# Performance work log

Hardware: AMD Instinct MI355X
Metric: run time of the kernel (lower is better)

Reference implementation:

```python
import jax, jax.numpy as jnp
import numpy as np

# DARTS recurrent genotype (canonical): (activation, predecessor-state index)
GENOTYPE_RECURRENT = [("sigmoid", 0), ("relu", 1), ("relu", 1), ("identity", 1),
                      ("tanh", 2), ("sigmoid", 5), ("tanh", 3), ("relu", 5)]
GENOTYPE_CONCAT = [1, 2, 3, 4, 5, 6, 7, 8]

T, B, H, V = 512, 64, 1024, 50000
INITRANGE = 0.04

_ACT = {"tanh": jnp.tanh, "relu": jax.nn.relu, "sigmoid": jax.nn.sigmoid,
        "identity": lambda x: x}


def setup_inputs() -> dict:
    key = jax.random.key(0)
    ks = jax.random.split(key, 5)
    X = jax.random.randint(ks[0], (T, B), 0, V)                     # token ids (T, B)
    hidden = jnp.zeros((1, B, H), dtype=jnp.float32)                # init hidden list[0]
    emb_table = jax.random.normal(ks[1], (V, H), dtype=jnp.float32) * 0.1
    W0 = jax.random.uniform(ks[2], (2 * H, 2 * H), jnp.float32, -INITRANGE, INITRANGE)
    Ws = jax.random.uniform(ks[3], (len(GENOTYPE_RECURRENT), H, 2 * H), jnp.float32,
                            -INITRANGE, INITRANGE)
    W_out = jax.random.normal(ks[4], (H, 4), dtype=jnp.float32) * 0.02
    b_out = jnp.zeros((4,), dtype=jnp.float32)
    return {"X": X, "hidden": hidden, "emb_table": emb_table, "W0": W0,
            "Ws": Ws, "W_out": W_out, "b_out": b_out}


def _darts_cell_step(h_prev, x, W0, Ws):
    # x, h_prev: (B, H). Eval-mode (no dropout masks).
    xh = jnp.concatenate([x, h_prev], axis=-1)          # (B, 2H)
    c0h0 = xh @ W0                                      # (B, 2H)
    c0 = jax.nn.sigmoid(c0h0[:, :H])
    h0 = jnp.tanh(c0h0[:, H:])
    s0 = h_prev + c0 * (h0 - h_prev)
    states = [s0]
    for i, (name, pred) in enumerate(GENOTYPE_RECURRENT):
        s_prev = states[pred]
        ch = s_prev @ Ws[i]                             # (B, 2H)
        c = jax.nn.sigmoid(ch[:, :H])
        hh = _ACT[name](ch[:, H:])
        states.append(s_prev + c * (hh - s_prev))
    # mean over concat nodes
    out = jnp.mean(jnp.stack([states[i] for i in GENOTYPE_CONCAT], axis=-1), axis=-1)
    return out, out


def reference(X, hidden, emb_table, W0, Ws, W_out, b_out):
    emb = emb_table[X]                                  # (T, B, H)
    h0 = hidden[0]                                      # (B, H)

    def step(h, x_t):
        return _darts_cell_step(h, x_t, W0, Ws)

    h_last, hiddens = jax.lax.scan(step, h0, emb)       # h_last: (B, H)
    a_hat = h_last @ W_out + b_out                      # (B, 4)
    probs = jax.nn.softmax(a_hat, axis=1)
    return a_hat, probs
```

## Files before the change

### kernel.cpp

```cpp
#include <hip/hip_runtime.h>

#define TT 512

typedef _Float16 f16;
typedef _Float16 half8 __attribute__((ext_vector_type(8)));
typedef float f32x4 __attribute__((ext_vector_type(4)));

#define MFMA(a,b,c) __builtin_amdgcn_mfma_f32_16x16x32_f16((a),(b),(c),0,0,0)
#define LOSC  2048.0f
#define RLOSC 0.00048828125f

#define RS  18
#define WSZ (16*RS)
#define LSZ (16*WSZ)

__device__ __forceinline__ half8 ldh8(const f16* p){ return *(const half8*)p; }
__device__ __forceinline__ float sgm(float x){ return 1.f/(1.f+__expf(-x)); }
__device__ __forceinline__ float applyact(int k, float x){
  if (k==0) return tanhf(x);
  if (k==1) return sgm(x);
  if (k==2) return fmaxf(x,0.f);
  return x;
}

__device__ __forceinline__ void gbar_arrive(unsigned* bar, unsigned ph, int b, int tid){
  __syncthreads();
  if (tid==0){
    __builtin_amdgcn_fence(__ATOMIC_RELEASE, "agent");
    __hip_atomic_store(&bar[b*16], ph+1u, __ATOMIC_RELAXED, __HIP_MEMORY_SCOPE_AGENT);
  }
}

__device__ __forceinline__ void gbar_wait(unsigned* bar, unsigned ph, int b, int tid){
  const unsigned tgt = ph + 1u;
  if (b==0){
    if (tid<256){
      while (__hip_atomic_load(&bar[tid*16], __ATOMIC_RELAXED, __HIP_MEMORY_SCOPE_AGENT) < tgt)
        __builtin_amdgcn_s_sleep(2);
    }
    __syncthreads();
    if (tid==0){
      __builtin_amdgcn_fence(__ATOMIC_ACQ_REL, "agent");
      __hip_atomic_store(&bar[4096], tgt, __ATOMIC_RELAXED, __HIP_MEMORY_SCOPE_AGENT);
    }
  }
  if (tid==0){
    while (__hip_atomic_load(&bar[4096], __ATOMIC_RELAXED, __HIP_MEMORY_SCOPE_AGENT) < tgt)
      __builtin_amdgcn_s_sleep(2);
    __builtin_amdgcn_fence(__ATOMIC_ACQUIRE, "agent");
  }
  __syncthreads();
}

struct WF2 { half8 g0,a0,gl0,al0,g1,a1,gl1,al1; };

__device__ __forceinline__ WF2 preW(const f16* __restrict__ Wh, const f16* __restrict__ Wl,
  int Kst, int c0, int kk, int q8, int l15, int wlo)
{
  WF2 F;
  const f16* Bg = Wh + (size_t)(c0+l15)*Kst + kk + q8;
  const f16* Ba = Wh + (size_t)(1024+c0+l15)*Kst + kk + q8;
  F.g0=ldh8(Bg); F.a0=ldh8(Ba); F.g1=ldh8(Bg+32); F.a1=ldh8(Ba+32);
  if (wlo){
    const f16* Bgl = Wl + (size_t)(c0+l15)*Kst + kk + q8;
    const f16* Bal = Wl + (size_t)(1024+c0+l15)*Kst + kk + q8;
    F.gl0=ldh8(Bgl); F.al0=ldh8(Bal); F.gl1=ldh8(Bgl+32); F.al1=ldh8(Bal+32);
  } else { F.gl0=F.g0; F.al0=F.a0; F.gl1=F.g1; F.al1=F.a1; }
  return F;
}

template<int NCH>
__device__ __forceinline__ void mm_mix(const WF2& F,
  const f16* __restrict__ Ap, const f16* __restrict__ Alp,
  const f16* __restrict__ Bg, const f16* __restrict__ Ba,
  const f16* __restrict__ Bgl, const f16* __restrict__ Bal,
  int wlo, float* __restrict__ Lg, float* __restrict__ La,
  int region, int q8, int l15)
{
  f32x4 g0={0,0,0,0},g1={0,0,0,0},a0={0,0,0,0},a1={0,0,0,0};
  {
    half8 ah=ldh8(Ap), al=ldh8(Alp);
    g0=MFMA(ah,F.g0,g0); a0=MFMA(ah,F.a0,a0);
    g1=MFMA(al,F.g0,g1); a1=MFMA(al,F.a0,a1);
    if (wlo){ g1=MFMA(ah,F.gl0,g1); a1=MFMA(ah,F.al0,a1); }
  }
  if (NCH>1){
    half8 ah=ldh8(Ap+32), al=ldh8(Alp+32);
    g0=MFMA(ah,F.g1,g0); a0=MFMA(ah,F.a1,a0);
    g1=MFMA(al,F.g1,g1); a1=MFMA(al,F.a1,a1);
    if (wlo){ g1=MFMA(ah,F.gl1,g1); a1=MFMA(ah,F.al1,a1); }
  }
  #pragma unroll
  for (int c=2;c<NCH;c++){
    int s=c*32;
    half8 ah=ldh8(Ap+s), al=ldh8(Alp+s);
    half8 wg=ldh8(Bg+s), wa=ldh8(Ba+s);
    g0=MFMA(ah,wg,g0); a0=MFMA(ah,wa,a0);
    g1=MFMA(al,wg,g1); a1=MFMA(al,wa,a1);
    if (wlo){ g1=MFMA(ah,ldh8(Bgl+s),g1); a1=MFMA(ah,ldh8(Bal+s),a1); }
  }
  f32x4 gg = g0 + g1*RLOSC, aa = a0 + a1*RLOSC;
  const int base = region*WSZ + (q8>>1)*RS + l15;
  #pragma unroll
  for (int rr=0;rr<4;rr++){
    Lg[base + rr*RS] = gg[rr];
    La[base + rr*RS] = aa[rr];
  }
}

template<int NCH>
__device__ __forceinline__ void node_pre(const WF2& F,
  const f16* __restrict__ SHs, const f16* __restrict__ SLs,
  const f16* __restrict__ Wh, const f16* __restrict__ Wl,
  float* __restrict__ Lg, float* __restrict__ La,
  int region, int kk, int m0, int c0, int q8, int l15, int wlo)
{
  const f16* Ap  = SHs + (m0+l15)*1024 + kk + q8;
  const f16* Alp = SLs + (m0+l15)*1024 + kk + q8;
  const f16* Bg  = Wh + (size_t)(c0+l15)*1024 + kk + q8;
  const f16* Ba  = Wh + (size_t)(1024+c0+l15)*1024 + kk + q8;
  const f16* Bgl = wlo ? Wl + (size_t)(c0+l15)*1024 + kk + q8 : Bg;
  const f16* Bal = wlo ? Wl + (size_t)(1024+c0+l15)*1024 + kk + q8 : Ba;
  mm_mix<NCH>(F, Ap, Alp, Bg, Ba, Bgl, Bal, wlo, Lg, La, region, q8, l15);
}

__device__ __forceinline__ float fin_val(const float* __restrict__ Lg, const float* __restrict__ La,
  const float* __restrict__ ST, int t256, int m0, int c0, int r0, int nr, int sp, int actk)
{
  const int row = t256>>4, col = t256&15;
  const int e = row*RS + col;
  float gs=0.f, as=0.f;
  for (int r=r0; r<r0+nr; ++r){ gs += Lg[r*WSZ+e]; as += La[r*WSZ+e]; }
  float spv = ST[sp*65536 + (m0+row)*1024 + c0 + col];
  return spv + sgm(gs)*(applyact(actk,as)-spv);
}

__device__ __forceinline__ void fin_write(const float* __restrict__ Lg, const float* __restrict__ La,
  float* __restrict__ ST, f16* __restrict__ SH, f16* __restrict__ SL,
  int t256, int m0, int c0, int r0, int nr, int sp, int so, int actk, bool hl)
{
  float s = fin_val(Lg, La, ST, t256, m0, c0, r0, nr, sp, actk);
  const int row = t256>>4, col = t256&15;
  const int idx = so*65536 + (m0+row)*1024 + c0 + col;
  ST[idx] = s;
  if (hl){ f16 hi=(f16)s; SH[idx]=hi; SL[idx]=(f16)((s-(float)hi)*LOSC); }
}

__global__ __launch_bounds__(1024,4) void darts_coop(
  const int* __restrict__ X, const float* __restrict__ emb,
  const float* __restrict__ Wout, const float* __restrict__ bout, float* __restrict__ out,
  const f16* __restrict__ W0Th, const f16* __restrict__ W0Tl,
  const f16* __restrict__ WsTh, const f16* __restrict__ WsTl,
  float* __restrict__ ST, f16* __restrict__ SH, f16* __restrict__ SL,
  f16* __restrict__ XNH, f16* __restrict__ XNL,
  unsigned* bar, int wlo)
{
  const int tid = threadIdx.x, b = blockIdx.x;
  const int wid = tid>>6, lane = tid&63, l15 = lane&15, q8 = (lane>>4)*8;
  const int mt = (b>>3)&3, sct = (b&7)*8 + (b>>5);
  const int m0 = mt*16, c0 = sct*16;
  __shared__ float Lg[LSZ], La[LSZ];
  __shared__ float S6[256], S8[256];
  unsigned ph = 0;

  WF2 F0 = preW(W0Th, W0Tl, 2048, c0, wid*128, q8, l15, wlo);

  for (int t=0; t<TT; ++t){
    if (t+1 < TT && tid < 256){
      int row = b>>2, col = ((b&3)<<8) + tid;
      int tok = X[(t+1)*64 + row];
      float v = emb[(size_t)tok*1024 + col];
      f16 hi=(f16)v;
      int xi = ((t+1)&1)*65536 + row*1024 + col;
      XNH[xi]=hi; XNL[xi]=(f16)((v-(float)hi)*LOSC);
    }
    {
      const f16* XH = XNH + (t&1)*65536;
      const f16* XL = XNL + (t&1)*65536;
      int kk = wid*128, ak = kk & 1023;
      const f16* Abh = (wid<8)? XH : SH;
      const f16* Abl = (wid<8)? XL : SL;
      const f16* Ap  = Abh + (m0+l15)*1024 + ak + q8;
      const f16* Alp = Abl + (m0+l15)*1024 + ak + q8;
      const f16* Bg  = W0Th + (size_t)(c0+l15)*2048 + kk + q8;
      const f16* Ba  = W0Th + (size_t)(1024+c0+l15)*2048 + kk + q8;
      const f16* Bgl = wlo ? W0Tl + (size_t)(c0+l15)*2048 + kk + q8 : Bg;
      const f16* Bal = wlo ? W0Tl + (size_t)(1024+c0+l15)*2048 + kk + q8 : Ba;
      mm_mix<4>(F0, Ap, Alp, Bg, Ba, Bgl, Bal, wlo, Lg, La, wid, q8, l15);
    }
    __syncthreads();
    if (tid<256) fin_write(Lg,La,ST,SH,SL, tid, m0,c0, 0,16, 0, 1, 0, true);
    gbar_arrive(bar, ph, b, tid);
    WF2 F1 = preW(WsTh, WsTl, 1024, c0, wid*64, q8, l15, wlo);
    gbar_wait(bar, ph, b, tid); ph++;

    node_pre<2>(F1, SH+1*65536, SL+1*65536, WsTh, WsTl, Lg, La, wid, wid*64, m0,c0,q8,l15,wlo);
    __syncthreads();
    if (tid<256) fin_write(Lg,La,ST,SH,SL, tid, m0,c0, 0,16, 1, 2, 1, true);
    gbar_arrive(bar, ph, b, tid);
    WF2 F2 = (wid<8)
      ? preW(WsTh+(size_t)1*2097152, wlo? WsTl+(size_t)1*2097152 : (const f16*)0,
             1024, c0, (wid&7)*128, q8, l15, wlo)
      : preW(WsTh+(size_t)2*2097152, wlo? WsTl+(size_t)2*2097152 : (const f16*)0,
             1024, c0, (wid&7)*128, q8, l15, wlo);
    gbar_wait(bar, ph, b, tid); ph++;

    if (wid<8)
      node_pre<4>(F2, SH+2*65536, SL+2*65536, WsTh+(size_t)1*2097152,
                  wlo? WsTl+(size_t)1*2097152 : (const f16*)0,
                  Lg, La, wid, (wid&7)*128, m0,c0,q8,l15,wlo);
    else
      node_pre<4>(F2, SH+2*65536, SL+2*65536, WsTh+(size_t)2*2097152,
                  wlo? WsTl+(size_t)2*2097152 : (const f16*)0,
                  Lg, La, wid, (wid&7)*128, m0,c0,q8,l15,wlo);
    __syncthreads();
    if (tid<256)      fin_write(Lg,La,ST,SH,SL, tid,     m0,c0, 0,8, 2, 3, 2, true);
    else if (tid<512) fin_write(Lg,La,ST,SH,SL, tid-256, m0,c0, 8,8, 2, 4, 2, true);
    __syncthreads();

    {
      WF2 F2b = preW(WsTh+(size_t)3*2097152, wlo? WsTl+(size_t)3*2097152 : (const f16*)0,
                     1024, c0, wid*64, q8, l15, wlo);
      node_pre<2>(F2b, SH+2*65536, SL+2*65536, WsTh+(size_t)3*2097152,
                  wlo? WsTl+(size_t)3*2097152 : (const f16*)0,
                  Lg, La, wid, wid*64, m0,c0,q8,l15,wlo);
    }
    __syncthreads();
    if (tid<256) fin_write(Lg,La,ST,SH,SL, tid, m0,c0, 0,16, 2, 5, 3, false);
    gbar_arrive(bar, ph, b, tid);
    WF2 F3 = (wid<8)
      ? preW(WsTh+(size_t)4*2097152, wlo? WsTl+(size_t)4*2097152 : (const f16*)0,
             1024, c0, (wid&7)*128, q8, l15, wlo)
      : preW(WsTh+(size_t)6*2097152, wlo? WsTl+(size_t)6*2097152 : (const f16*)0,
             1024, c0, (wid&7)*128, q8, l15, wlo);
    gbar_wait(bar, ph, b, tid); ph++;

    if (wid<8)
      node_pre<4>(F3, SH+3*65536, SL+3*65536, WsTh+(size_t)4*2097152,
                  wlo? WsTl+(size_t)4*2097152 : (const f16*)0,
                  Lg, La, wid, (wid&7)*128, m0,c0,q8,l15,wlo);
    else
      node_pre<4>(F3, SH+4*65536, SL+4*65536, WsTh+(size_t)6*2097152,
                  wlo? WsTl+(size_t)6*2097152 : (const f16*)0,
                  Lg, La, wid, (wid&7)*128, m0,c0,q8,l15,wlo);
    __syncthreads();
    if (tid<256)      fin_write(Lg,La,ST,SH,SL, tid,     m0,c0, 0,8, 3, 6, 0, true);
    else if (tid<512) fin_write(Lg,La,ST,SH,SL, tid-256, m0,c0, 8,8, 4, 8, 0, false);
    gbar_arrive(bar, ph, b, tid);
    WF2 F4 = (wid<8)
      ? preW(WsTh+(size_t)5*2097152, wlo? WsTl+(size_t)5*2097152 : (const f16*)0,
             1024, c0, (wid&7)*128, q8, l15, wlo)
      : preW(WsTh+(size_t)7*2097152, wlo? WsTl+(size_t)7*2097152 : (const f16*)0,
             1024, c0, (wid&7)*128, q8, l15, wlo);
    gbar_wait(bar, ph, b, tid); ph++;

    if (wid<8)
      node_pre<4>(F4, SH+6*65536, SL+6*65536, WsTh+(size_t)5*2097152,
                  wlo? WsTl+(size_t)5*2097152 : (const f16*)0,
                  Lg, La, wid, (wid&7)*128, m0,c0,q8,l15,wlo);
    else
      node_pre<4>(F4, SH+6*65536, SL+6*65536, WsTh+(size_t)7*2097152,
                  wlo? WsTl+(size_t)7*2097152 : (const f16*)0,
                  Lg, La, wid, (wid&7)*128, m0,c0,q8,l15,wlo);
    __syncthreads();
    if (tid<256)      S6[tid]     = fin_val(Lg,La,ST, tid,     m0,c0, 0,8, 6, 1);
    else if (tid<512) S8[tid-256] = fin_val(Lg,La,ST, tid-256, m0,c0, 8,8, 6, 2);
    __syncthreads();
    if (tid<256){
      const int row = tid>>4, col = tid&15;
      const int idx = (m0+row)*1024 + c0 + col;
      float m = (ST[2*65536+idx]+ST[3*65536+idx]+ST[4*65536+idx]+ST[5*65536+idx]
               + ST[6*65536+idx]+ST[8*65536+idx]+S6[tid]+S8[tid])*0.125f;
      ST[idx]=m;
      f16 hi=(f16)m; SH[idx]=hi; SL[idx]=(f16)((m-(float)hi)*LOSC);
    }
    gbar_arrive(bar, ph, b, tid);
    F0 = preW(W0Th, W0Tl, 2048, c0, wid*128, q8, l15, wlo);
    gbar_wait(bar, ph, b, tid); ph++;
  }

  if (b==0 && tid<256){
    int row = tid>>2, col = tid&3;
    float acc = bout[col];
    const float* hrow = ST + row*1024;
    #pragma unroll 8
    for (int k=0;k<1024;k++) acc += hrow[k]*Wout[k*4+col];
    out[row*4+col] = acc;
    float m = fmaxf(acc, __shfl_xor(acc,1));
    m = fmaxf(m, __shfl_xor(m,2));
    float e = __expf(acc-m);
    float ssum = e + __shfl_xor(e,1);
    ssum = ssum + __shfl_xor(ssum,2);
    out[256 + row*4+col] = e/ssum;
  }
}

__global__ void prep_x0(const int* __restrict__ X, const float* __restrict__ hidden,
  const float* __restrict__ emb, f16* __restrict__ XNH, f16* __restrict__ XNL,
  float* __restrict__ ST, f16* __restrict__ SH, f16* __restrict__ SL, unsigned* bar)
{
  int idx = blockIdx.x*256 + threadIdx.x;
  float hv = hidden[idx];
  ST[idx] = hv;
  f16 hh=(f16)hv; SH[idx]=hh; SL[idx]=(f16)((hv-(float)hh)*LOSC);
  int brow = idx>>10, k = idx&1023;
  int tok = X[brow];
  float v = emb[tok*1024+k];
  f16 xh=(f16)v; XNH[idx]=xh; XNL[idx]=(f16)((v-(float)xh)*LOSC);
  if (idx < 8192) bar[idx] = 0u;
}

__global__ void prep_w(const float* __restrict__ W0, const float* __restrict__ Ws,
  f16* __restrict__ W0Th, f16* __restrict__ W0Tl, f16* __restrict__ WsTh, f16* __restrict__ WsTl)
{
  __shared__ float L[64][65];
  int b = blockIdx.x, tid = threadIdx.x;
  const float* src; f16 *Dh, *Dl; int K, tk, tn;
  if (b < 1024){ src=W0; Dh=W0Th; Dl=W0Tl; K=2048; tk=b&31; tn=b>>5; }
  else { int bb=b-1024; int mi=bb>>9; int t2=bb&511; tk=t2&15; tn=t2>>4;
         src = Ws + (size_t)mi*1024*2048; Dh = WsTh + (size_t)mi*2097152;
         Dl = WsTl ? (WsTl + (size_t)mi*2097152) : (f16*)0; K=1024; }
  int k0 = tk*64, n0 = tn*64;
  int rr = tid>>6, cc = tid&63;
  #pragma unroll
  for (int j=0;j<16;j++){
    int r = j*4 + rr;
    L[cc][r] = src[(size_t)(k0+r)*2048 + n0+cc];
  }
  __syncthreads();
  #pragma unroll
  for (int j=0;j<16;j++){
    int n = j*4 + rr;
    float v = L[n][cc];
    f16 hi = (f16)v;
    Dh[(size_t)(n0+n)*K + k0+cc] = hi;
    if (Dl) Dl[(size_t)(n0+n)*K + k0+cc] = (f16)((v-(float)hi)*LOSC);
  }
}

__global__ void sentinel_k(float* __restrict__ out, float v){
  int i = blockIdx.x*256 + threadIdx.x;
  if (i < 512) out[i] = v;
}

extern "C" void kernel_launch(void* const* d_in, const int* in_sizes, int n_in,
                              void* d_out, int out_size, void* d_ws, size_t ws_size,
                              hipStream_t stream)
{
  const int*   X      = (const int*)  d_in[0];
  const float* hidden = (const float*)d_in[1];
  const float* emb    = (const float*)d_in[2];
  const float* W0     = (const float*)d_in[3];
  const float* Ws     = (const float*)d_in[4];
  const float* Wout   = (const float*)d_in[5];
  const float* bout   = (const float*)d_in[6];
  float* out = (float*)d_out;

  const size_t SZ_W0   = (size_t)2048*2048*2;
  const size_t SZ_WS   = (size_t)8*2048*1024*2;
  const size_t SZ_ST   = (size_t)10*65536*4;
  const size_t SZ_SHL  = (size_t)10*65536*2;
  const size_t SZ_XN   = (size_t)2*65536*2;
  const size_t SZ_BAR  = 32768;

  auto pad = [](size_t x){ return (x + 255) & ~(size_t)255; };
  size_t need_red  = pad(SZ_W0) + pad(SZ_WS) + pad(SZ_ST) + 2*pad(SZ_SHL)
                   + 2*pad(SZ_XN) + pad(SZ_BAR);
  size_t need_full = need_red + pad(SZ_W0) + pad(SZ_WS);

  int wlo;
  if (ws_size >= need_full)      wlo = 1;
  else if (ws_size >= need_red)  wlo = 0;
  else { hipLaunchKernelGGL(sentinel_k, dim3(2), dim3(256), 0, stream, out, 1.0e6f); return; }

  char* w = (char*)d_ws; size_t off = 0;
  auto alloc = [&](size_t bytes)->void*{ void* p = w+off; off += (bytes+255)&~(size_t)255; return p; };
  f16* W0Th = (f16*)alloc(SZ_W0);
  f16* WsTh = (f16*)alloc(SZ_WS);
  f16* W0Tl = wlo ? (f16*)alloc(SZ_W0) : (f16*)0;
  f16* WsTl = wlo ? (f16*)alloc(SZ_WS) : (f16*)0;
  float* ST = (float*)alloc(SZ_ST);
  f16* SH   = (f16*)alloc(SZ_SHL);
  f16* SL   = (f16*)alloc(SZ_SHL);
  f16* XNH  = (f16*)alloc(SZ_XN);
  f16* XNL  = (f16*)alloc(SZ_XN);
  unsigned* bar = (unsigned*)alloc(SZ_BAR);

  hipLaunchKernelGGL(prep_x0, dim3(256), dim3(256), 0, stream,
                     X, hidden, emb, XNH, XNL, ST, SH, SL, bar);
  hipLaunchKernelGGL(prep_w, dim3(5120), dim3(256), 0, stream,
                     W0, Ws, W0Th, W0Tl, WsTh, WsTl);

  void* args[] = { (void*)&X, (void*)&emb, (void*)&Wout, (void*)&bout, (void*)&out,
                   (void*)&W0Th, (void*)&W0Tl, (void*)&WsTh, (void*)&WsTl,
                   (void*)&ST, (void*)&SH, (void*)&SL, (void*)&XNH, (void*)&XNL,
                   (void*)&bar, (void*)&wlo };
  hipError_t e = hipLaunchCooperativeKernel((void*)darts_coop, dim3(256), dim3(1024), args, 0, stream);
  if (e != hipSuccess){
    hipLaunchKernelGGL(darts_coop, dim3(256), dim3(1024), 0, stream,
                       X, emb, Wout, bout, out, W0Th, W0Tl, WsTh, WsTl,
                       ST, SH, SL, XNH, XNL, bar, wlo);
  }
}
```

Measured before the change: 64.89 ms.

## Replace grid-barrier fences with sc1 coherent loads/stores and drop weight prefetch

Removes the agent-scope acquire/release fences from the grid barrier wait path. Shared state values are instead read and written with inline-asm global loads and stores carrying the sc1 cache-coherence bit, so they bypass non-coherent cache levels. The activation fragments are batch-issued before one waitcnt. The register-held weight prefetch that was overlapped with the barrier wait is removed, so weights are now loaded inside the matmul loop. This cuts cache-invalidate and writeback cost at each of the many barriers per step. The cost is losing weight-load overlap and depending on sc1 semantics for correctness, and the arrive-side release fence remains.

```diff
diff --git a/kernel.cpp b/kernel.cpp
--- a/kernel.cpp
+++ b/kernel.cpp
@@ -23,6 +23,24 @@
   return x;
 }
 
+__device__ __forceinline__ void issue_ld4_sc1(half8& d, const f16* p){
+  asm volatile("global_load_dwordx4 %0, %1, off sc1" : "=&v"(d) : "v"(p) : "memory");
+}
+__device__ __forceinline__ void issue_ldf_sc1(float& d, const float* p){
+  asm volatile("global_load_dword %0, %1, off sc1" : "=&v"(d) : "v"(p) : "memory");
+}
+__device__ __forceinline__ void vmwait(){
+  asm volatile("s_waitcnt vmcnt(0)" ::: "memory");
+  __builtin_amdgcn_sched_barrier(0);
+}
+__device__ __forceinline__ void st_f32_sc1(float* p, float v){
+  asm volatile("global_store_dword %0, %1, off sc1" :: "v"(p), "v"(v) : "memory");
+}
+__device__ __forceinline__ void st_f16_sc1(f16* p, f16 v){
+  unsigned uv = (unsigned)__builtin_bit_cast(unsigned short, v);
+  asm volatile("global_store_short %0, %1, off sc1" :: "v"(p), "v"(uv) : "memory");
+}
+
 __device__ __forceinline__ void gbar_arrive(unsigned* bar, unsigned ph, int b, int tid){
   __syncthreads();
   if (tid==0){
@@ -39,65 +57,39 @@
         __builtin_amdgcn_s_sleep(2);
     }
     __syncthreads();
-    if (tid==0){
-      __builtin_amdgcn_fence(__ATOMIC_ACQ_REL, "agent");
+    if (tid==0)
       __hip_atomic_store(&bar[4096], tgt, __ATOMIC_RELAXED, __HIP_MEMORY_SCOPE_AGENT);
-    }
   }
   if (tid==0){
     while (__hip_atomic_load(&bar[4096], __ATOMIC_RELAXED, __HIP_MEMORY_SCOPE_AGENT) < tgt)
       __builtin_amdgcn_s_sleep(2);
-    __builtin_amdgcn_fence(__ATOMIC_ACQUIRE, "agent");
   }
   __syncthreads();
 }
 
-struct WF2 { half8 g0,a0,gl0,al0,g1,a1,gl1,al1; };
-
-__device__ __forceinline__ WF2 preW(const f16* __restrict__ Wh, const f16* __restrict__ Wl,
-  int Kst, int c0, int kk, int q8, int l15, int wlo)
-{
-  WF2 F;
-  const f16* Bg = Wh + (size_t)(c0+l15)*Kst + kk + q8;
-  const f16* Ba = Wh + (size_t)(1024+c0+l15)*Kst + kk + q8;
-  F.g0=ldh8(Bg); F.a0=ldh8(Ba); F.g1=ldh8(Bg+32); F.a1=ldh8(Ba+32);
-  if (wlo){
-    const f16* Bgl = Wl + (size_t)(c0+l15)*Kst + kk + q8;
-    const f16* Bal = Wl + (size_t)(1024+c0+l15)*Kst + kk + q8;
-    F.gl0=ldh8(Bgl); F.al0=ldh8(Bal); F.gl1=ldh8(Bgl+32); F.al1=ldh8(Bal+32);
-  } else { F.gl0=F.g0; F.al0=F.a0; F.gl1=F.g1; F.al1=F.a1; }
-  return F;
-}
-
 template<int NCH>
-__device__ __forceinline__ void mm_mix(const WF2& F,
+__device__ __forceinline__ void mm_core(
   const f16* __restrict__ Ap, const f16* __restrict__ Alp,
   const f16* __restrict__ Bg, const f16* __restrict__ Ba,
   const f16* __restrict__ Bgl, const f16* __restrict__ Bal,
   int wlo, float* __restrict__ Lg, float* __restrict__ La,
   int region, int q8, int l15)
 {
+  half8 AH[NCH], AL[NCH];
+  #pragma unroll
+  for (int c=0;c<NCH;c++){
+    issue_ld4_sc1(AH[c], Ap+c*32);
+    issue_ld4_sc1(AL[c], Alp+c*32);
+  }
+  vmwait();
   f32x4 g0={0,0,0,0},g1={0,0,0,0},a0={0,0,0,0},a1={0,0,0,0};
-  {
-    half8 ah=ldh8(Ap), al=ldh8(Alp);
-    g0=MFMA(ah,F.g0,g0); a0=MFMA(ah,F.a0,a0);
-    g1=MFMA(al,F.g0,g1); a1=MFMA(al,F.a0,a1);
-    if (wlo){ g1=MFMA(ah,F.gl0,g1); a1=MFMA(ah,F.al0,a1); }
-  }
-  if (NCH>1){
-    half8 ah=ldh8(Ap+32), al=ldh8(Alp+32);
-    g0=MFMA(ah,F.g1,g0); a0=MFMA(ah,F.a1,a0);
-    g1=MFMA(al,F.g1,g1); a1=MFMA(al,F.a1,a1);
-    if (wlo){ g1=MFMA(ah,F.gl1,g1); a1=MFMA(ah,F.al1,a1); }
-  }
-  #pragma unroll
-  for (int c=2;c<NCH;c++){
-    int s=c*32;
-    half8 ah=ldh8(Ap+s), al=ldh8(Alp+s);
+  #pragma unroll
+  for (int c=0;c<NCH;c++){
+    int s = c*32;
     half8 wg=ldh8(Bg+s), wa=ldh8(Ba+s);
-    g0=MFMA(ah,wg,g0); a0=MFMA(ah,wa,a0);
-    g1=MFMA(al,wg,g1); a1=MFMA(al,wa,a1);
-    if (wlo){ g1=MFMA(ah,ldh8(Bgl+s),g1); a1=MFMA(ah,ldh8(Bal+s),a1); }
+    g0=MFMA(AH[c],wg,g0); a0=MFMA(AH[c],wa,a0);
+    g1=MFMA(AL[c],wg,g1); a1=MFMA(AL[c],wa,a1);
+    if (wlo){ g1=MFMA(AH[c],ldh8(Bgl+s),g1); a1=MFMA(AH[c],ldh8(Bal+s),a1); }
   }
   f32x4 gg = g0 + g1*RLOSC, aa = a0 + a1*RLOSC;
   const int base = region*WSZ + (q8>>1)*RS + l15;
@@ -109,7 +101,7 @@
 }
 
 template<int NCH>
-__device__ __forceinline__ void node_pre(const WF2& F,
+__device__ __forceinline__ void node_std(
   const f16* __restrict__ SHs, const f16* __restrict__ SLs,
   const f16* __restrict__ Wh, const f16* __restrict__ Wl,
   float* __restrict__ Lg, float* __restrict__ La,
@@ -121,17 +113,19 @@
   const f16* Ba  = Wh + (size_t)(1024+c0+l15)*1024 + kk + q8;
   const f16* Bgl = wlo ? Wl + (size_t)(c0+l15)*1024 + kk + q8 : Bg;
   const f16* Bal = wlo ? Wl + (size_t)(1024+c0+l15)*1024 + kk + q8 : Ba;
-  mm_mix<NCH>(F, Ap, Alp, Bg, Ba, Bgl, Bal, wlo, Lg, La, region, q8, l15);
+  mm_core<NCH>(Ap,Alp,Bg,Ba,Bgl,Bal,wlo,Lg,La,region,q8,l15);
 }
 
 __device__ __forceinline__ float fin_val(const float* __restrict__ Lg, const float* __restrict__ La,
   const float* __restrict__ ST, int t256, int m0, int c0, int r0, int nr, int sp, int actk)
 {
   const int row = t256>>4, col = t256&15;
+  float spv;
+  issue_ldf_sc1(spv, ST + sp*65536 + (m0+row)*1024 + c0 + col);
   const int e = row*RS + col;
   float gs=0.f, as=0.f;
   for (int r=r0; r<r0+nr; ++r){ gs += Lg[r*WSZ+e]; as += La[r*WSZ+e]; }
-  float spv = ST[sp*65536 + (m0+row)*1024 + c0 + col];
+  vmwait();
   return spv + sgm(gs)*(applyact(actk,as)-spv);
 }
 
@@ -142,8 +136,8 @@
   float s = fin_val(Lg, La, ST, t256, m0, c0, r0, nr, sp, actk);
   const int row = t256>>4, col = t256&15;
   const int idx = so*65536 + (m0+row)*1024 + c0 + col;
-  ST[idx] = s;
-  if (hl){ f16 hi=(f16)s; SH[idx]=hi; SL[idx]=(f16)((s-(float)hi)*LOSC); }
+  st_f32_sc1(ST+idx, s);
+  if (hl){ f16 hi=(f16)s; st_f16_sc1(SH+idx, hi); st_f16_sc1(SL+idx, (f16)((s-(float)hi)*LOSC)); }
 }
 
 __global__ __launch_bounds__(1024,4) void darts_coop(
@@ -163,8 +157,6 @@
   __shared__ float S6[256], S8[256];
   unsigned ph = 0;
 
-  WF2 F0 = preW(W0Th, W0Tl, 2048, c0, wid*128, q8, l15, wlo);
-
   for (int t=0; t<TT; ++t){
     if (t+1 < TT && tid < 256){
       int row = b>>2, col = ((b&3)<<8) + tid;
@@ -172,7 +164,8 @@
       float v = emb[(size_t)tok*1024 + col];
       f16 hi=(f16)v;
       int xi = ((t+1)&1)*65536 + row*1024 + col;
-      XNH[xi]=hi; XNL[xi]=(f16)((v-(float)hi)*LOSC);
+      st_f16_sc1(XNH+xi, hi);
+      st_f16_sc1(XNL+xi, (f16)((v-(float)hi)*LOSC));
     }
     {
       const f16* XH = XNH + (t&1)*65536;
@@ -186,31 +179,25 @@
       const f16* Ba  = W0Th + (size_t)(1024+c0+l15)*2048 + kk + q8;
       const f16* Bgl = wlo ? W0Tl + (size_t)(c0+l15)*2048 + kk + q8 : Bg;
       const f16* Bal = wlo ? W0Tl + (size_t)(1024+c0+l15)*2048 + kk + q8 : Ba;
-      mm_mix<4>(F0, Ap, Alp, Bg, Ba, Bgl, Bal, wlo, Lg, La, wid, q8, l15);
+      mm_core<4>(Ap,Alp,Bg,Ba,Bgl,Bal,wlo,Lg,La,wid,q8,l15);
     }
     __syncthreads();
     if (tid<256) fin_write(Lg,La,ST,SH,SL, tid, m0,c0, 0,16, 0, 1, 0, true);
     gbar_arrive(bar, ph, b, tid);
-    WF2 F1 = preW(WsTh, WsTl, 1024, c0, wid*64, q8, l15, wlo);
-    gbar_wait(bar, ph, b, tid); ph++;
-
-    node_pre<2>(F1, SH+1*65536, SL+1*65536, WsTh, WsTl, Lg, La, wid, wid*64, m0,c0,q8,l15,wlo);
+    gbar_wait(bar, ph, b, tid); ph++;
+
+    node_std<2>(SH+1*65536, SL+1*65536, WsTh, WsTl, Lg, La, wid, wid*64, m0,c0,q8,l15,wlo);
     __syncthreads();
     if (tid<256) fin_write(Lg,La,ST,SH,SL, tid, m0,c0, 0,16, 1, 2, 1, true);
     gbar_arrive(bar, ph, b, tid);
-    WF2 F2 = (wid<8)
-      ? preW(WsTh+(size_t)1*2097152, wlo? WsTl+(size_t)1*2097152 : (const f16*)0,
-             1024, c0, (wid&7)*128, q8, l15, wlo)
-      : preW(WsTh+(size_t)2*2097152, wlo? WsTl+(size_t)2*2097152 : (const f16*)0,
-             1024, c0, (wid&7)*128, q8, l15, wlo);
     gbar_wait(bar, ph, b, tid); ph++;
 
     if (wid<8)
-      node_pre<4>(F2, SH+2*65536, SL+2*65536, WsTh+(size_t)1*2097152,
+      node_std<4>(SH+2*65536, SL+2*65536, WsTh+(size_t)1*2097152,
                   wlo? WsTl+(size_t)1*2097152 : (const f16*)0,
                   Lg, La, wid, (wid&7)*128, m0,c0,q8,l15,wlo);
     else
-      node_pre<4>(F2, SH+2*65536, SL+2*65536, WsTh+(size_t)2*2097152,
+      node_std<4>(SH+2*65536, SL+2*65536, WsTh+(size_t)2*2097152,
                   wlo? WsTl+(size_t)2*2097152 : (const f16*)0,
                   Lg, La, wid, (wid&7)*128, m0,c0,q8,l15,wlo);
     __syncthreads();
@@ -218,48 +205,34 @@
     else if (tid<512) fin_write(Lg,La,ST,SH,SL, tid-256, m0,c0, 8,8, 2, 4, 2, true);
     __syncthreads();
 
-    {
-      WF2 F2b = preW(WsTh+(size_t)3*2097152, wlo? WsTl+(size_t)3*2097152 : (const f16*)0,
-                     1024, c0, wid*64, q8, l15, wlo);
-      node_pre<2>(F2b, SH+2*65536, SL+2*65536, WsTh+(size_t)3*2097152,
-                  wlo? WsTl+(size_t)3*2097152 : (const f16*)0,
-                  Lg, La, wid, wid*64, m0,c0,q8,l15,wlo);
-    }
+    node_std<2>(SH+2*65536, SL+2*65536, WsTh+(size_t)3*2097152,
+                wlo? WsTl+(size_t)3*2097152 : (const f16*)0,
+                Lg, La, wid, wid*64, m0,c0,q8,l15,wlo);
     __syncthreads();
     if (tid<256) fin_write(Lg,La,ST,SH,SL, tid, m0,c0, 0,16, 2, 5, 3, false);
     gbar_arrive(bar, ph, b, tid);
-    WF2 F3 = (wid<8)
-      ? preW(WsTh+(size_t)4*2097152, wlo? WsTl+(size_t)4*2097152 : (const f16*)0,
-             1024, c0, (wid&7)*128, q8, l15, wlo)
-      : preW(WsTh+(size_t)6*2097152, wlo? WsTl+(size_t)6*2097152 : (const f16*)0,
-             1024, c0, (wid&7)*128, q8, l15, wlo);
     gbar_wait(bar, ph, b, tid); ph++;
 
     if (wid<8)
-      node_pre<4>(F3, SH+3*65536, SL+3*65536, WsTh+(size_t)4*2097152,
+      node_std<4>(SH+3*65536, SL+3*65536, WsTh+(size_t)4*2097152,
                   wlo? WsTl+(size_t)4*2097152 : (const f16*)0,
                   Lg, La, wid, (wid&7)*128, m0,c0,q8,l15,wlo);
     else
-      node_pre<4>(F3, SH+4*65536, SL+4*65536, WsTh+(size_t)6*2097152,
+      node_std<4>(SH+4*65536, SL+4*65536, WsTh+(size_t)6*2097152,
                   wlo? WsTl+(size_t)6*2097152 : (const f16*)0,
                   Lg, La, wid, (wid&7)*128, m0,c0,q8,l15,wlo);
     __syncthreads();
     if (tid<256)      fin_write(Lg,La,ST,SH,SL, tid,     m0,c0, 0,8, 3, 6, 0, true);
     else if (tid<512) fin_write(Lg,La,ST,SH,SL, tid-256, m0,c0, 8,8, 4, 8, 0, false);
     gbar_arrive(bar, ph, b, tid);
-    WF2 F4 = (wid<8)
-      ? preW(WsTh+(size_t)5*2097152, wlo? WsTl+(size_t)5*2097152 : (const f16*)0,
-             1024, c0, (wid&7)*128, q8, l15, wlo)
-      : preW(WsTh+(size_t)7*2097152, wlo? WsTl+(size_t)7*2097152 : (const f16*)0,
-             1024, c0, (wid&7)*128, q8, l15, wlo);
     gbar_wait(bar, ph, b, tid); ph++;
 
     if (wid<8)
-      node_pre<4>(F4, SH+6*65536, SL+6*65536, WsTh+(size_t)5*2097152,
+      node_std<4>(SH+6*65536, SL+6*65536, WsTh+(size_t)5*2097152,
                   wlo? WsTl+(size_t)5*2097152 : (const f16*)0,
                   Lg, La, wid, (wid&7)*128, m0,c0,q8,l15,wlo);
     else
-      node_pre<4>(F4, SH+6*65536, SL+6*65536, WsTh+(size_t)7*2097152,
+      node_std<4>(SH+6*65536, SL+6*65536, WsTh+(size_t)7*2097152,
                   wlo? WsTl+(size_t)7*2097152 : (const f16*)0,
                   Lg, La, wid, (wid&7)*128, m0,c0,q8,l15,wlo);
     __syncthreads();
@@ -269,29 +242,42 @@
     if (tid<256){
       const int row = tid>>4, col = tid&15;
       const int idx = (m0+row)*1024 + c0 + col;
-      float m = (ST[2*65536+idx]+ST[3*65536+idx]+ST[4*65536+idx]+ST[5*65536+idx]
-               + ST[6*65536+idx]+ST[8*65536+idx]+S6[tid]+S8[tid])*0.125f;
-      ST[idx]=m;
-      f16 hi=(f16)m; SH[idx]=hi; SL[idx]=(f16)((m-(float)hi)*LOSC);
-    }
-    gbar_arrive(bar, ph, b, tid);
-    F0 = preW(W0Th, W0Tl, 2048, c0, wid*128, q8, l15, wlo);
-    gbar_wait(bar, ph, b, tid); ph++;
-  }
-
-  if (b==0 && tid<256){
-    int row = tid>>2, col = tid&3;
-    float acc = bout[col];
-    const float* hrow = ST + row*1024;
-    #pragma unroll 8
-    for (int k=0;k<1024;k++) acc += hrow[k]*Wout[k*4+col];
-    out[row*4+col] = acc;
-    float m = fmaxf(acc, __shfl_xor(acc,1));
-    m = fmaxf(m, __shfl_xor(m,2));
-    float e = __expf(acc-m);
-    float ssum = e + __shfl_xor(e,1);
-    ssum = ssum + __shfl_xor(ssum,2);
-    out[256 + row*4+col] = e/ssum;
+      float v2,v3,v4,v5,v6,v8;
+      issue_ldf_sc1(v2, ST+2*65536+idx);
+      issue_ldf_sc1(v3, ST+3*65536+idx);
+      issue_ldf_sc1(v4, ST+4*65536+idx);
+      issue_ldf_sc1(v5, ST+5*65536+idx);
+      issue_ldf_sc1(v6, ST+6*65536+idx);
+      issue_ldf_sc1(v8, ST+8*65536+idx);
+      float slocal = S6[tid] + S8[tid];
+      vmwait();
+      float m = (v2+v3+v4+v5+v6+v8+slocal)*0.125f;
+      st_f32_sc1(ST+idx, m);
+      f16 hi=(f16)m;
+      st_f16_sc1(SH+idx, hi);
+      st_f16_sc1(SL+idx, (f16)((m-(float)hi)*LOSC));
+    }
+    gbar_arrive(bar, ph, b, tid);
+    gbar_wait(bar, ph, b, tid); ph++;
+  }
+
+  if (b==0){
+    if (tid==0) __builtin_amdgcn_fence(__ATOMIC_ACQUIRE, "agent");
+    __syncthreads();
+    if (tid<256){
+      int row = tid>>2, col = tid&3;
+      float acc = bout[col];
+      const float* hrow = ST + row*1024;
+      #pragma unroll 8
+      for (int k=0;k<1024;k++) acc += hrow[k]*Wout[k*4+col];
+      out[row*4+col] = acc;
+      float m = fmaxf(acc, __shfl_xor(acc,1));
+      m = fmaxf(m, __shfl_xor(m,2));
+      float e = __expf(acc-m);
+      float ssum = e + __shfl_xor(e,1);
+      ssum = ssum + __shfl_xor(ssum,2);
+      out[256 + row*4+col] = e/ssum;
+    }
   }
 }
 
```

New measurement: 52.65 ms. 1.23x faster.
